# Optimization experiments

Measured on AMD Instinct MI355X. Metric: run time of the kernel, lower is better.

The kernel has to match this reference:

```python
import jax, jax.numpy as jnp
import numpy as np

LAMBDA_COE = 0.5
EPS = 1e-12  # F.normalize default eps


def setup_inputs() -> dict:
    key = jax.random.key(0)
    k1, k2, k3 = jax.random.split(key, 3)
    B, C = 8192, 2
    D, N = 1024, 8192
    outputs = jax.random.normal(k1, (B, C), dtype=jnp.float32)
    labels = jax.random.randint(k2, (B,), 0, C, dtype=jnp.int64)
    H = jax.random.normal(k3, (D, N), dtype=jnp.float32)
    return {"outputs": outputs, "labels": labels, "H": H}


def reference(outputs, labels, H):
    # --- pairwise cosine-similarity regularizer over columns of H ---
    Ht = H.T                                   # [N, D]
    N = Ht.shape[0]
    norms = jnp.maximum(jnp.linalg.norm(Ht, axis=1, keepdims=True), EPS)
    Hn = Ht / norms                            # row-normalized [N, D]
    G = Hn @ Hn.T                              # [N, N] cosine sims
    # sum over strict upper triangle = (sum(G) - trace(G)) / 2
    pair_sum = (jnp.sum(G) - jnp.trace(G)) * 0.5
    reg_term = pair_sum * LAMBDA_COE / (N * (N - 1) / 2)

    # --- cross-entropy (mean reduction), matching nn.CrossEntropyLoss ---
    logp = jax.nn.log_softmax(outputs, axis=-1)          # [B, C]
    nll = -jnp.take_along_axis(logp, labels[:, None], axis=1)[:, 0]
    ce = jnp.mean(nll)

    return ce + reg_term
```

## Files before the change

### kernel.cpp

```cpp
#include <hip/hip_runtime.h>
#include <math.h>


#define N_COLS  8192
#define D_ROWS  1024
#define B_ROWS  8192
#define CSS_BLOCKS   256
#define CSS_ROWS_PER  32
#define CE_BLOCKS    32
#define GEMV_BLOCKS  1024

__device__ inline float block_reduce_sum_256(float v) {
    #pragma unroll
    for (int off = 32; off > 0; off >>= 1) v += __shfl_down(v, off, 64);
    __shared__ float sm[4];
    int lane = threadIdx.x & 63;
    int wid  = threadIdx.x >> 6;
    if (lane == 0) sm[wid] = v;
    __syncthreads();
    if (threadIdx.x < 4) {
        v = sm[threadIdx.x];
        v += __shfl_down(v, 2, 64);
        v += __shfl_down(v, 1, 64);
    }
    return v;
}

__global__ __launch_bounds__(256)
void colsumsq_ce_kernel(const float* __restrict__ H,
                        const float* __restrict__ logits,
                        const int* __restrict__ labels,
                        float* __restrict__ norms2,
                        float* __restrict__ ce_acc) {
    if (blockIdx.x < CSS_BLOCKS) {
        const int cg = blockIdx.x & 7;
        const int rg = blockIdx.x >> 3;
        const int col4 = cg * 256 + threadIdx.x;
        const int row0 = rg * CSS_ROWS_PER;
        const float4* __restrict__ H4 = (const float4*)H;
        float ax = 0.f, ay = 0.f, az = 0.f, aw = 0.f;
        #pragma unroll
        for (int r = 0; r < CSS_ROWS_PER; ++r) {
            float4 v = H4[(size_t)(row0 + r) * (N_COLS / 4) + col4];
            ax = fmaf(v.x, v.x, ax);
            ay = fmaf(v.y, v.y, ay);
            az = fmaf(v.z, v.z, az);
            aw = fmaf(v.w, v.w, aw);
        }
        const int col = col4 * 4;
        atomicAdd(&norms2[col + 0], ax);
        atomicAdd(&norms2[col + 1], ay);
        atomicAdd(&norms2[col + 2], az);
        atomicAdd(&norms2[col + 3], aw);
    } else {
        const int b = (blockIdx.x - CSS_BLOCKS) * 256 + threadIdx.x;
        float2 x = ((const float2*)logits)[b];
        float m = fmaxf(x.x, x.y);
        float lse = m + __logf(__expf(x.x - m) + __expf(x.y - m));
        float xl = (labels[b] == 0) ? x.x : x.y;
        float s = block_reduce_sum_256(lse - xl);
        if (threadIdx.x == 0) atomicAdd(ce_acc, s);
    }
}

__global__ __launch_bounds__(256)
void gemv_s2_finalize_kernel(const float* __restrict__ H,
                             const float* __restrict__ norms2,
                             float* __restrict__ s2_acc,
                             const float* __restrict__ ce_acc,
                             unsigned int* __restrict__ done_cnt,
                             float* __restrict__ out) {
    const int d = blockIdx.x;
    const float4* __restrict__ Hrow = (const float4*)(H + (size_t)d * N_COLS);
    const float4* __restrict__ n24  = (const float4*)norms2;
    float acc = 0.f;
    #pragma unroll
    for (int i = threadIdx.x; i < N_COLS / 4; i += 256) {
        float4 v  = Hrow[i];
        float4 n2 = n24[i];
        acc = fmaf(v.x, rsqrtf(fmaxf(n2.x, 1e-24f)), acc);
        acc = fmaf(v.y, rsqrtf(fmaxf(n2.y, 1e-24f)), acc);
        acc = fmaf(v.z, rsqrtf(fmaxf(n2.z, 1e-24f)), acc);
        acc = fmaf(v.w, rsqrtf(fmaxf(n2.w, 1e-24f)), acc);
    }
    float s = block_reduce_sum_256(acc);
    __shared__ bool last;
    if (threadIdx.x == 0) {
        atomicAdd(s2_acc, s * s);
        __threadfence();
        unsigned int old = atomicAdd(done_cnt, 1u);
        last = (old == GEMV_BLOCKS - 1);
    }
    __syncthreads();
    if (last && threadIdx.x == 0) {
        float s2 = atomicAdd(s2_acc, 0.f);
        float ce = atomicAdd((float*)ce_acc, 0.f);
        double reg = ((double)s2 - (double)N_COLS) * 0.5
                     / ((double)N_COLS * (double)(N_COLS - 1));
        out[0] = (float)((double)ce / (double)B_ROWS + reg);
    }
}

extern "C" void kernel_launch(void* const* d_in, const int* in_sizes, int n_in,
                              void* d_out, int out_size, void* d_ws, size_t ws_size,
                              hipStream_t stream) {
    const float* outputs = (const float*)d_in[0];
    const int*   labels  = (const int*)d_in[1];
    const float* H       = (const float*)d_in[2];
    float* out = (float*)d_out;

    float* norms2 = (float*)d_ws;
    float* s2_acc = norms2 + N_COLS;
    float* ce_acc = s2_acc + 1;
    unsigned int* done_cnt = (unsigned int*)(ce_acc + 1);

    hipMemsetAsync(d_ws, 0, (N_COLS + 3) * sizeof(float), stream);

    colsumsq_ce_kernel<<<CSS_BLOCKS + CE_BLOCKS, 256, 0, stream>>>(
        H, outputs, labels, norms2, ce_acc);
    gemv_s2_finalize_kernel<<<GEMV_BLOCKS, 256, 0, stream>>>(
        H, norms2, s2_acc, ce_acc, done_cnt, out);
}
```

Before: 117.2 us.

## Fuse column-norm, GEMV and finalize into one persistent kernel with grid barriers

Merges the two kernels into a single 256-block kernel. Each block computes column sum-of-squares for its 32x1024 tile, then waits at a global atomic-counter barrier and re-reads the same tile to form the normalized row sums, reducing per wavefront into per-row atomics. Block 0 then waits on a second counter and computes the final squared sum plus cross-entropy. This removes a launch and aims to serve the second pass over H from cache, at the cost of spin barriers that depend on all 256 blocks being resident at once and many more fine-grained atomics.

```diff
diff --git a/kernel.cpp b/kernel.cpp
--- a/kernel.cpp
+++ b/kernel.cpp
@@ -2,13 +2,11 @@
 #include <math.h>
 
 
-#define N_COLS  8192
-#define D_ROWS  1024
-#define B_ROWS  8192
-#define CSS_BLOCKS   256
-#define CSS_ROWS_PER  32
-#define CE_BLOCKS    32
-#define GEMV_BLOCKS  1024
+#define N_COLS 8192
+#define D_ROWS 1024
+#define B_ROWS 8192
+#define NBLK   256
+#define EPSQ   1e-24f
 
 __device__ inline float block_reduce_sum_256(float v) {
     #pragma unroll
@@ -27,74 +25,90 @@
 }
 
 __global__ __launch_bounds__(256)
-void colsumsq_ce_kernel(const float* __restrict__ H,
-                        const float* __restrict__ logits,
-                        const int* __restrict__ labels,
-                        float* __restrict__ norms2,
-                        float* __restrict__ ce_acc) {
-    if (blockIdx.x < CSS_BLOCKS) {
-        const int cg = blockIdx.x & 7;
-        const int rg = blockIdx.x >> 3;
-        const int col4 = cg * 256 + threadIdx.x;
-        const int row0 = rg * CSS_ROWS_PER;
-        const float4* __restrict__ H4 = (const float4*)H;
-        float ax = 0.f, ay = 0.f, az = 0.f, aw = 0.f;
-        #pragma unroll
-        for (int r = 0; r < CSS_ROWS_PER; ++r) {
-            float4 v = H4[(size_t)(row0 + r) * (N_COLS / 4) + col4];
-            ax = fmaf(v.x, v.x, ax);
-            ay = fmaf(v.y, v.y, ay);
-            az = fmaf(v.z, v.z, az);
-            aw = fmaf(v.w, v.w, aw);
-        }
-        const int col = col4 * 4;
-        atomicAdd(&norms2[col + 0], ax);
-        atomicAdd(&norms2[col + 1], ay);
-        atomicAdd(&norms2[col + 2], az);
-        atomicAdd(&norms2[col + 3], aw);
-    } else {
-        const int b = (blockIdx.x - CSS_BLOCKS) * 256 + threadIdx.x;
-        float2 x = ((const float2*)logits)[b];
+void fused_kernel(const float* __restrict__ H,
+                  const float* __restrict__ logits,
+                  const int* __restrict__ labels,
+                  float* __restrict__ norms2,
+                  float* __restrict__ s_vec,
+                  float* __restrict__ ce_acc,
+                  unsigned int* __restrict__ sync_ctr,
+                  float* __restrict__ out) {
+    const int b = blockIdx.x, t = threadIdx.x;
+    const int cg = b & 7;
+    const int rg = b >> 3;
+    const int col4 = cg * 256 + t;
+    const float4* __restrict__ H4 = (const float4*)H;
+
+    float ax = 0.f, ay = 0.f, az = 0.f, aw = 0.f;
+    #pragma unroll 16
+    for (int r = 0; r < 32; ++r) {
+        float4 v = H4[(size_t)(rg * 32 + r) * (N_COLS / 4) + col4];
+        ax = fmaf(v.x, v.x, ax);
+        ay = fmaf(v.y, v.y, ay);
+        az = fmaf(v.z, v.z, az);
+        aw = fmaf(v.w, v.w, aw);
+    }
+    atomicAdd(&norms2[col4 * 4 + 0], ax);
+    atomicAdd(&norms2[col4 * 4 + 1], ay);
+    atomicAdd(&norms2[col4 * 4 + 2], az);
+    atomicAdd(&norms2[col4 * 4 + 3], aw);
+
+    float nll = 0.f;
+    if (t < 32) {
+        const int row = b * 32 + t;
+        float2 x = ((const float2*)logits)[row];
         float m = fmaxf(x.x, x.y);
         float lse = m + __logf(__expf(x.x - m) + __expf(x.y - m));
-        float xl = (labels[b] == 0) ? x.x : x.y;
-        float s = block_reduce_sum_256(lse - xl);
-        if (threadIdx.x == 0) atomicAdd(ce_acc, s);
+        nll = lse - ((labels[row] == 0) ? x.x : x.y);
     }
-}
+    if (t < 64) {
+        #pragma unroll
+        for (int off = 16; off > 0; off >>= 1) nll += __shfl_down(nll, off, 64);
+        if (t == 0) atomicAdd(ce_acc, nll);
+    }
 
-__global__ __launch_bounds__(256)
-void gemv_s2_finalize_kernel(const float* __restrict__ H,
-                             const float* __restrict__ norms2,
-                             float* __restrict__ s2_acc,
-                             const float* __restrict__ ce_acc,
-                             unsigned int* __restrict__ done_cnt,
-                             float* __restrict__ out) {
-    const int d = blockIdx.x;
-    const float4* __restrict__ Hrow = (const float4*)(H + (size_t)d * N_COLS);
-    const float4* __restrict__ n24  = (const float4*)norms2;
-    float acc = 0.f;
-    #pragma unroll
-    for (int i = threadIdx.x; i < N_COLS / 4; i += 256) {
-        float4 v  = Hrow[i];
-        float4 n2 = n24[i];
-        acc = fmaf(v.x, rsqrtf(fmaxf(n2.x, 1e-24f)), acc);
-        acc = fmaf(v.y, rsqrtf(fmaxf(n2.y, 1e-24f)), acc);
-        acc = fmaf(v.z, rsqrtf(fmaxf(n2.z, 1e-24f)), acc);
-        acc = fmaf(v.w, rsqrtf(fmaxf(n2.w, 1e-24f)), acc);
-    }
-    float s = block_reduce_sum_256(acc);
-    __shared__ bool last;
-    if (threadIdx.x == 0) {
-        atomicAdd(s2_acc, s * s);
-        __threadfence();
-        unsigned int old = atomicAdd(done_cnt, 1u);
-        last = (old == GEMV_BLOCKS - 1);
+    __threadfence();
+    __syncthreads();
+    if (t == 0) {
+        atomicAdd(&sync_ctr[0], 1u);
+        while (atomicAdd(&sync_ctr[0], 0u) < NBLK) __builtin_amdgcn_s_sleep(1);
     }
     __syncthreads();
-    if (last && threadIdx.x == 0) {
-        float s2 = atomicAdd(s2_acc, 0.f);
-        float ce = atomicAdd((float*)ce_acc, 0.f);
+    __threadfence();
+
+    float4 n2 = ((const float4*)norms2)[col4];
+    const float wx = rsqrtf(fmaxf(n2.x, EPSQ));
+    const float wy = rsqrtf(fmaxf(n2.y, EPSQ));
+    const float wz = rsqrtf(fmaxf(n2.z, EPSQ));
+    const float ww = rsqrtf(fmaxf(n2.w, EPSQ));
+    #pragma unroll 8
+    for (int r = 0; r < 32; ++r) {
+        float4 v = H4[(size_t)(rg * 32 + r) * (N_COLS / 4) + col4];
+        float p = fmaf(v.x, wx, fmaf(v.y, wy, fmaf(v.z, wz, v.w * ww)));
+        #pragma unroll
+        for (int off = 32; off > 0; off >>= 1) p += __shfl_down(p, off, 64);
+        if ((t & 63) == 0) atomicAdd(&s_vec[rg * 32 + r], p);
+    }
+
+    __threadfence();
+    __syncthreads();
+    if (t == 0) atomicAdd(&sync_ctr[1], 1u);
+    if (b != 0) return;
+    if (t == 0) {
+        while (atomicAdd(&sync_ctr[1], 0u) < NBLK) __builtin_amdgcn_s_sleep(1);
+    }
+    __syncthreads();
+    __threadfence();
+
+    float sq = 0.f;
+    #pragma unroll
+    for (int i = 0; i < 4; ++i) {
+        float s = s_vec[t + i * 256];
+        sq = fmaf(s, s, sq);
+    }
+    float s2 = block_reduce_sum_256(sq);
+    if (t == 0) {
+        float ce = *(volatile float*)ce_acc;
         double reg = ((double)s2 - (double)N_COLS) * 0.5
                      / ((double)N_COLS * (double)(N_COLS - 1));
         out[0] = (float)((double)ce / (double)B_ROWS + reg);
@@ -110,14 +124,13 @@
     float* out = (float*)d_out;
 
     float* norms2 = (float*)d_ws;
-    float* s2_acc = norms2 + N_COLS;
-    float* ce_acc = s2_acc + 1;
-    unsigned int* done_cnt = (unsigned int*)(ce_acc + 1);
+    float* s_vec  = norms2 + N_COLS;
+    float* ce_acc = s_vec + D_ROWS;
+    unsigned int* sync_ctr = (unsigned int*)(ce_acc + 8);
 
-    hipMemsetAsync(d_ws, 0, (N_COLS + 3) * sizeof(float), stream);
+    const size_t zero_bytes = (N_COLS + D_ROWS + 8 + 2) * sizeof(float);
+    hipMemsetAsync(d_ws, 0, zero_bytes, stream);
 
-    colsumsq_ce_kernel<<<CSS_BLOCKS + CE_BLOCKS, 256, 0, stream>>>(
-        H, outputs, labels, norms2, ce_acc);
-    gemv_s2_finalize_kernel<<<GEMV_BLOCKS, 256, 0, stream>>>(
-        H, norms2, s2_acc, ce_acc, done_cnt, out);
+    fused_kernel<<<NBLK, 256, 0, stream>>>(H, outputs, labels,
+                                           norms2, s_vec, ce_acc, sync_ctr, out);
 }
```

Result: slower. 183.5 us (+56.5%).

## Split GEMV rows across two blocks and double column-norm blocks

Applied to the files above, without the earlier changes.

The column sum-of-squares pass now uses 512 blocks of 16 rows each instead of 256 blocks of 32 rows. The GEMV pass splits each row of H across two blocks and accumulates per-row partial sums into a workspace vector with per-wave atomics. The last block then squares and sums that vector itself, since squaring must happen after both halves are summed. The aim is more parallelism for the bandwidth-bound reads of H, at the cost of more atomics and a larger final reduction.

```diff
diff --git a/kernel.cpp b/kernel.cpp
--- a/kernel.cpp
+++ b/kernel.cpp
@@ -2,13 +2,13 @@
 #include <math.h>
 
 
-#define N_COLS  8192
-#define D_ROWS  1024
-#define B_ROWS  8192
-#define CSS_BLOCKS   256
-#define CSS_ROWS_PER  32
-#define CE_BLOCKS    32
-#define GEMV_BLOCKS  1024
+#define N_COLS 8192
+#define D_ROWS 1024
+#define B_ROWS 8192
+#define CSS_BLOCKS 512
+#define CE_BLOCKS  32
+#define GEMV_BLOCKS (D_ROWS * 2)
+#define EPSQ 1e-24f
 
 __device__ inline float block_reduce_sum_256(float v) {
     #pragma unroll
@@ -32,15 +32,16 @@
                         const int* __restrict__ labels,
                         float* __restrict__ norms2,
                         float* __restrict__ ce_acc) {
+    const int t = threadIdx.x;
     if (blockIdx.x < CSS_BLOCKS) {
         const int cg = blockIdx.x & 7;
         const int rg = blockIdx.x >> 3;
-        const int col4 = cg * 256 + threadIdx.x;
-        const int row0 = rg * CSS_ROWS_PER;
+        const int col4 = cg * 256 + t;
+        const int row0 = rg * 16;
         const float4* __restrict__ H4 = (const float4*)H;
         float ax = 0.f, ay = 0.f, az = 0.f, aw = 0.f;
         #pragma unroll
-        for (int r = 0; r < CSS_ROWS_PER; ++r) {
+        for (int r = 0; r < 16; ++r) {
             float4 v = H4[(size_t)(row0 + r) * (N_COLS / 4) + col4];
             ax = fmaf(v.x, v.x, ax);
             ay = fmaf(v.y, v.y, ay);
@@ -53,48 +54,62 @@
         atomicAdd(&norms2[col + 2], az);
         atomicAdd(&norms2[col + 3], aw);
     } else {
-        const int b = (blockIdx.x - CSS_BLOCKS) * 256 + threadIdx.x;
+        const int b = (blockIdx.x - CSS_BLOCKS) * 256 + t;
         float2 x = ((const float2*)logits)[b];
         float m = fmaxf(x.x, x.y);
         float lse = m + __logf(__expf(x.x - m) + __expf(x.y - m));
-        float xl = (labels[b] == 0) ? x.x : x.y;
-        float s = block_reduce_sum_256(lse - xl);
-        if (threadIdx.x == 0) atomicAdd(ce_acc, s);
+        float s = block_reduce_sum_256(lse - ((labels[b] == 0) ? x.x : x.y));
+        if (t == 0) atomicAdd(ce_acc, s);
     }
 }
 
 __global__ __launch_bounds__(256)
-void gemv_s2_finalize_kernel(const float* __restrict__ H,
-                             const float* __restrict__ norms2,
-                             float* __restrict__ s2_acc,
-                             const float* __restrict__ ce_acc,
-                             unsigned int* __restrict__ done_cnt,
-                             float* __restrict__ out) {
-    const int d = blockIdx.x;
+void gemv_finalize_kernel(const float* __restrict__ H,
+                          const float* __restrict__ norms2,
+                          float* __restrict__ s_vec,
+                          const float* __restrict__ ce_acc,
+                          unsigned int* __restrict__ done_cnt,
+                          float* __restrict__ out) {
+    const int t = threadIdx.x;
+    const int d = blockIdx.x >> 1;
+    const int h = blockIdx.x & 1;
     const float4* __restrict__ Hrow = (const float4*)(H + (size_t)d * N_COLS);
     const float4* __restrict__ n24  = (const float4*)norms2;
-    float acc = 0.f;
+    float p = 0.f;
     #pragma unroll
-    for (int i = threadIdx.x; i < N_COLS / 4; i += 256) {
+    for (int k = 0; k < 4; ++k) {
+        const int i = h * 1024 + k * 256 + t;
         float4 v  = Hrow[i];
         float4 n2 = n24[i];
-        acc = fmaf(v.x, rsqrtf(fmaxf(n2.x, 1e-24f)), acc);
-        acc = fmaf(v.y, rsqrtf(fmaxf(n2.y, 1e-24f)), acc);
-        acc = fmaf(v.z, rsqrtf(fmaxf(n2.z, 1e-24f)), acc);
-        acc = fmaf(v.w, rsqrtf(fmaxf(n2.w, 1e-24f)), acc);
+        p = fmaf(v.x, rsqrtf(fmaxf(n2.x, EPSQ)), p);
+        p = fmaf(v.y, rsqrtf(fmaxf(n2.y, EPSQ)), p);
+        p = fmaf(v.z, rsqrtf(fmaxf(n2.z, EPSQ)), p);
+        p = fmaf(v.w, rsqrtf(fmaxf(n2.w, EPSQ)), p);
     }
-    float s = block_reduce_sum_256(acc);
+    #pragma unroll
+    for (int off = 32; off > 0; off >>= 1) p += __shfl_down(p, off, 64);
+    if ((t & 63) == 0) atomicAdd(&s_vec[d], p);
+
+    __threadfence();
+    __syncthreads();
     __shared__ bool last;
-    if (threadIdx.x == 0) {
-        atomicAdd(s2_acc, s * s);
-        __threadfence();
+    if (t == 0) {
         unsigned int old = atomicAdd(done_cnt, 1u);
         last = (old == GEMV_BLOCKS - 1);
     }
     __syncthreads();
-    if (last && threadIdx.x == 0) {
-        float s2 = atomicAdd(s2_acc, 0.f);
-        float ce = atomicAdd((float*)ce_acc, 0.f);
+    if (!last) return;
+    __threadfence();
+
+    float sq = 0.f;
+    #pragma unroll
+    for (int i = 0; i < 4; ++i) {
+        float s = s_vec[t + i * 256];
+        sq = fmaf(s, s, sq);
+    }
+    float s2 = block_reduce_sum_256(sq);
+    if (t == 0) {
+        float ce = *(volatile float*)ce_acc;
         double reg = ((double)s2 - (double)N_COLS) * 0.5
                      / ((double)N_COLS * (double)(N_COLS - 1));
         out[0] = (float)((double)ce / (double)B_ROWS + reg);
@@ -110,14 +125,14 @@
     float* out = (float*)d_out;
 
     float* norms2 = (float*)d_ws;
-    float* s2_acc = norms2 + N_COLS;
-    float* ce_acc = s2_acc + 1;
-    unsigned int* done_cnt = (unsigned int*)(ce_acc + 1);
+    float* s_vec  = norms2 + N_COLS;
+    float* ce_acc = s_vec + D_ROWS;
+    unsigned int* done_cnt = (unsigned int*)(ce_acc + 8);
 
-    hipMemsetAsync(d_ws, 0, (N_COLS + 3) * sizeof(float), stream);
+    hipMemsetAsync(d_ws, 0, (N_COLS + D_ROWS + 16) * sizeof(float), stream);
 
     colsumsq_ce_kernel<<<CSS_BLOCKS + CE_BLOCKS, 256, 0, stream>>>(
         H, outputs, labels, norms2, ce_acc);
-    gemv_s2_finalize_kernel<<<GEMV_BLOCKS, 256, 0, stream>>>(
-        H, norms2, s2_acc, ce_acc, done_cnt, out);
+    gemv_finalize_kernel<<<GEMV_BLOCKS, 256, 0, stream>>>(
+        H, norms2, s_vec, ce_acc, done_cnt, out);
 }
```

Result: slower. 264.7 us (+125.8%).
